# Optimization experiments

Measured on AMD Instinct MI355X. Metric: run time of the kernel, lower is better.

The kernel has to match this reference:

```python
import jax, jax.numpy as jnp
import numpy as np

D_MODEL = 768
N_HEADS = 12
D_K = D_MODEL // N_HEADS
NEG_INF = -1e10


def setup_inputs() -> dict:
    key = jax.random.key(0)
    ks = jax.random.split(key, 12)
    B, S = 2, 4096
    scale = 1.0 / np.sqrt(D_MODEL)
    inp = {
        "q": jax.random.normal(ks[0], (B, S, D_MODEL), jnp.float32),
        "k": jax.random.normal(ks[1], (B, S, D_MODEL), jnp.float32),
        "v": jax.random.normal(ks[2], (B, S, D_MODEL), jnp.float32),
        "mask": jnp.ones((B, S), jnp.int32),
        "Wq": jax.random.normal(ks[3], (D_MODEL, D_MODEL), jnp.float32) * scale,
        "bq": jnp.zeros((D_MODEL,), jnp.float32),
        "Wk": jax.random.normal(ks[4], (D_MODEL, D_MODEL), jnp.float32) * scale,
        "bk": jnp.zeros((D_MODEL,), jnp.float32),
        "Wv": jax.random.normal(ks[5], (D_MODEL, D_MODEL), jnp.float32) * scale,
        "bv": jnp.zeros((D_MODEL,), jnp.float32),
        "Wo": jax.random.normal(ks[6], (D_MODEL, D_MODEL), jnp.float32) * scale,
        "bo": jnp.zeros((D_MODEL,), jnp.float32),
    }
    return inp


def reference(q, k, v, mask, Wq, bq, Wk, bk, Wv, bv, Wo, bo):
    B, Sq, _ = q.shape
    Sk = k.shape[1]
    # linear projections (flax Linear: x @ kernel + bias)
    query = q @ Wq + bq
    key_ = k @ Wk + bk
    value = v @ Wv + bv
    # split heads: [B, H, S, d_k]
    query = query.reshape(B, Sq, N_HEADS, D_K).transpose(0, 2, 1, 3)
    key_ = key_.reshape(B, Sk, N_HEADS, D_K).transpose(0, 2, 1, 3)
    value = value.reshape(B, Sk, N_HEADS, D_K).transpose(0, 2, 1, 3)
    # scores [B, H, Sq, Sk]
    scores = jnp.einsum('bhqd,bhkd->bhqk', query, key_) / jnp.sqrt(
        jnp.asarray(D_K, query.dtype))
    m = mask[:, None, None, :]  # 2D mask -> [B,1,1,Sk]
    scores = jnp.where(m == 0, NEG_INF, scores)
    attn = jax.nn.softmax(scores, axis=-1)
    # dropout deterministic (is_training=False): identity
    x = jnp.einsum('bhqk,bhkd->bhqd', attn, value)
    x = x.transpose(0, 2, 1, 3).reshape(B, Sq, D_MODEL)
    return x @ Wo + bo
```

## Files before the change

### kernel.cpp

```cpp
#include <hip/hip_runtime.h>

typedef __attribute__((ext_vector_type(8))) short short8;
typedef __attribute__((ext_vector_type(4))) float floatx4;
typedef __attribute__((ext_vector_type(16))) float floatx16;
typedef unsigned short ushort_t;

#define S_LEN 4096
#define NH 12
#define DK 64
#define DM 768
#define BQ 128
#define LOG2E 1.4426950408889634f

static __device__ __forceinline__ unsigned short f2bf(float f) {
    unsigned int u = __float_as_uint(f);
    u += 0x7FFFu + ((u >> 16) & 1u);
    return (unsigned short)(u >> 16);
}
static __device__ __forceinline__ unsigned pack2(float a, float b) {
    return (unsigned)f2bf(a) | ((unsigned)f2bf(b) << 16);
}
static __device__ __forceinline__ void gld_lds16(const void* g, void* l) {
    __builtin_amdgcn_global_load_lds(
        (__attribute__((address_space(1))) void*)g,
        (__attribute__((address_space(3))) void*)l, 16, 0, 0);
}

__global__ __launch_bounds__(256)
void wtrans_kernel(const float* __restrict__ W0, const float* __restrict__ W1,
                   const float* __restrict__ W2, const float* __restrict__ W3,
                   ushort_t* __restrict__ T0, ushort_t* __restrict__ T1,
                   ushort_t* __restrict__ T2, ushort_t* __restrict__ T3) {
    __shared__ float tile[32][33];
    const int z = blockIdx.z;
    const float* W = (z == 0) ? W0 : (z == 1) ? W1 : (z == 2) ? W2 : W3;
    ushort_t* T = (z == 0) ? T0 : (z == 1) ? T1 : (z == 2) ? T2 : T3;
    const int bx = blockIdx.x, by = blockIdx.y;
    const int tx = threadIdx.x, ty = threadIdx.y;
    #pragma unroll
    for (int j = 0; j < 32; j += 8)
        tile[ty + j][tx] = W[(size_t)(by * 32 + ty + j) * DM + bx * 32 + tx];
    __syncthreads();
    #pragma unroll
    for (int j = 0; j < 32; j += 8)
        T[(size_t)(bx * 32 + ty + j) * DM + by * 32 + tx] = f2bf(tile[tx][ty + j]);
}

__global__ __launch_bounds__(256)
void cvt_kernel(const float* __restrict__ A0, const float* __restrict__ A1,
                const float* __restrict__ A2, ushort_t* __restrict__ O0,
                ushort_t* __restrict__ O1, ushort_t* __restrict__ O2) {
    const int z = blockIdx.y;
    const float* A = (z == 0) ? A0 : (z == 1) ? A1 : A2;
    ushort_t* O = (z == 0) ? O0 : (z == 1) ? O1 : O2;
    const size_t i = ((size_t)blockIdx.x * 256 + threadIdx.x) * 8;
    const float4 f0 = *(const float4*)(A + i);
    const float4 f1 = *(const float4*)(A + i + 4);
    uint4 o;
    o.x = pack2(f0.x, f0.y);
    o.y = pack2(f0.z, f0.w);
    o.z = pack2(f1.x, f1.y);
    o.w = pack2(f1.z, f1.w);
    *(uint4*)(O + i) = o;
}

__global__ __launch_bounds__(256)
void vtrans_kernel(const ushort_t* __restrict__ Vn, ushort_t* __restrict__ Vt) {
    __shared__ ushort_t tl[64 * 72];
    const int s0 = blockIdx.x * 64;
    const size_t bh = blockIdx.y;
    const int t = threadIdx.x;
    {
        const int r = t >> 2, c0 = (t & 3) * 16;
        const uint4* src = (const uint4*)(Vn + (bh * S_LEN + s0 + r) * DK + c0);
        uint4 a0 = src[0], a1 = src[1];
        uint4* dst = (uint4*)&tl[r * 72 + c0];
        dst[0] = a0;
        dst[1] = a1;
    }
    __syncthreads();
    {
        const int d = t >> 2, c0 = (t & 3) * 16;
        alignas(16) ushort_t tmp[16];
        #pragma unroll
        for (int j = 0; j < 16; ++j) tmp[j] = tl[(c0 + j) * 72 + d];
        uint4* dst = (uint4*)(Vt + (bh * DK + d) * S_LEN + s0 + c0);
        dst[0] = *(const uint4*)&tmp[0];
        dst[1] = *(const uint4*)&tmp[8];
    }
}

struct GemmArgs {
    const ushort_t* A[3];
    const ushort_t* Wt[3];
    const float* bias[3];
    void* C[3];
    float scale[3];
};

template <int MODE>
__global__ __launch_bounds__(256, 3)
void gemm_kernel(GemmArgs args) {
    __shared__ __align__(16) ushort_t As[128 * 64];
    __shared__ __align__(16) ushort_t Bs[128 * 64];
    const int z = blockIdx.z;
    const ushort_t* A = args.A[z];
    const ushort_t* Wt = args.Wt[z];
    const float* bias = args.bias[z];
    void* Carg = args.C[z];
    const float scale = args.scale[z];

    const int m0 = blockIdx.x * 128;
    const int n0 = blockIdx.y * 128;
    const int t = threadIdx.x;
    const int w = t >> 6, lane = t & 63, l15 = lane & 15, quad = lane >> 4;
    const int rowoff = (w >> 1) * 64, coloff = (w & 1) * 64;
    const int srow = w * 8 + (lane >> 3);
    const int schunk = lane & 7;
    const int gchunk = schunk ^ (lane >> 3);

    floatx4 acc[4][4];
    #pragma unroll
    for (int i = 0; i < 4; ++i)
        #pragma unroll
        for (int j = 0; j < 4; ++j) acc[i][j] = (floatx4){0.f, 0.f, 0.f, 0.f};

    for (int kt = 0; kt < DM; kt += 64) {
        __syncthreads();
        #pragma unroll
        for (int j = 0; j < 4; ++j) {
            const int r = j * 32 + srow;
            gld_lds16(A + (size_t)(m0 + r) * DM + kt + gchunk * 8,
                      &As[r * 64 + schunk * 8]);
        }
        #pragma unroll
        for (int j = 0; j < 4; ++j) {
            const int r = j * 32 + srow;
            gld_lds16(Wt + (size_t)(n0 + r) * DM + kt + gchunk * 8,
                      &Bs[r * 64 + schunk * 8]);
        }
        __asm__ __volatile__("s_waitcnt vmcnt(0)" ::: "memory");
        __syncthreads();

        #pragma unroll
        for (int kk = 0; kk < 2; ++kk) {
            short8 af[4], bfr[4];
            #pragma unroll
            for (int i = 0; i < 4; ++i) {
                const int r = rowoff + 16 * i + l15;
                af[i] = *(const short8*)&As[r * 64 + (((kk * 4 + quad) ^ (r & 7)) << 3)];
            }
            #pragma unroll
            for (int j = 0; j < 4; ++j) {
                const int r = coloff + 16 * j + l15;
                bfr[j] = *(const short8*)&Bs[r * 64 + (((kk * 4 + quad) ^ (r & 7)) << 3)];
            }
            #pragma unroll
            for (int i = 0; i < 4; ++i)
                #pragma unroll
                for (int j = 0; j < 4; ++j)
                    acc[i][j] = __builtin_amdgcn_mfma_f32_16x16x32_bf16(af[i], bfr[j], acc[i][j], 0, 0, 0);
        }
    }

    #pragma unroll
    for (int i = 0; i < 4; ++i) {
        #pragma unroll
        for (int j = 0; j < 4; ++j) {
            #pragma unroll
            for (int reg = 0; reg < 4; ++reg) {
                const int m = m0 + rowoff + 16 * i + quad * 4 + reg;
                const int n = n0 + coloff + 16 * j + l15;
                const float v2 = (acc[i][j][reg] + bias[n]) * scale;
                if (MODE == 0) {
                    ushort_t* Out = (ushort_t*)Carg;
                    const int b = m >> 12, s = m & 4095, h = n >> 6, d = n & 63;
                    Out[((size_t)((b * NH + h) * S_LEN + s)) * DK + d] = f2bf(v2);
                } else {
                    float* Out = (float*)Carg;
                    Out[(size_t)m * DM + n] = v2;
                }
            }
        }
    }
}

__global__ __launch_bounds__(256, 3)
void attn_kernel(const ushort_t* __restrict__ Q, const ushort_t* __restrict__ K,
                 const ushort_t* __restrict__ VT, const int* __restrict__ mask,
                 ushort_t* __restrict__ X) {
    __shared__ ushort_t Qs[BQ * DK];
    __shared__ ushort_t Ks0[64 * DK], Ks1[64 * DK];
    __shared__ ushort_t Vs0[64 * DK], Vs1[64 * DK];

    const int id = blockIdx.x;
    const int per = id >> 3;
    const int bh = (id & 7) * 3 + (per >> 5);
    const int qb = per & 31;
    const int b = bh / NH, h = bh - b * NH;
    const size_t bho = (size_t)bh * S_LEN;
    const ushort_t* Vbase = VT + (size_t)bh * DK * S_LEN;
    const int t = threadIdx.x;
    const int w = t >> 6, lane = t & 63, l31 = lane & 31, half = lane >> 5;
    const int q0 = qb * BQ;
    const int swl = l31 & 7;
    const int frow8 = lane >> 3;
    const int fcc = lane & 7;

    auto fillK = [&](int kv0, ushort_t* Kb) {
        #pragma unroll
        for (int j = 0; j < 2; ++j) {
            const int r = (w * 2 + j) * 8 + frow8;
            const int c8 = fcc ^ (r & 7);
            gld_lds16(K + (bho + kv0 + r) * DK + c8 * 8, &Kb[r * DK + fcc * 8]);
        }
    };
    auto fillV = [&](int kv0, ushort_t* Vb) {
        #pragma unroll
        for (int j = 0; j < 2; ++j) {
            const int r = (w * 2 + j) * 8 + frow8;
            const int c8 = fcc ^ (r & 7);
            gld_lds16(Vbase + (size_t)r * S_LEN + kv0 + c8 * 8, &Vb[r * DK + fcc * 8]);
        }
    };

    fillK(0, Ks0);
    fillV(0, Vs0);
    #pragma unroll
    for (int j = 0; j < 4; ++j) {
        const int r = (w * 4 + j) * 8 + frow8;
        const int c8 = fcc ^ (r & 7);
        gld_lds16(Q + (bho + q0 + r) * DK + c8 * 8, &Qs[r * DK + fcc * 8]);
    }
    int ok = 1;
    {
        const int* mrow = mask + (size_t)b * S_LEN + t * 16;
        #pragma unroll
        for (int i = 0; i < 4; ++i) {
            const int4 mm = *(const int4*)(mrow + i * 4);
            ok &= (mm.x != 0) & (mm.y != 0) & (mm.z != 0) & (mm.w != 0);
        }
    }
    const int allones = __syncthreads_and(ok);

    short8 qf[4];
    #pragma unroll
    for (int ks = 0; ks < 4; ++ks) {
        const int c8 = ks * 2 + half;
        qf[ks] = *(const short8*)&Qs[(w * 32 + l31) * DK + ((c8 ^ swl) << 3)];
    }

    floatx16 o[2];
    #pragma unroll
    for (int dt = 0; dt < 2; ++dt)
        #pragma unroll
        for (int r = 0; r < 16; ++r) o[dt][r] = 0.f;
    float l_r = 0.f;

    auto body = [&](int it, const ushort_t* Kc, const ushort_t* Vc,
                    ushort_t* Kn, ushort_t* Vn) {
        __syncthreads();
        if (it + 1 < S_LEN / 64) {
            fillK((it + 1) * 64, Kn);
            fillV((it + 1) * 64, Vn);
        }
        unsigned long long mb = ~0ULL;
        if (!allones) {
            const int mv = mask[(size_t)b * S_LEN + it * 64 + lane];
            mb = __ballot(mv != 0);
        }

        floatx16 st[2];
        __builtin_amdgcn_s_setprio(1);
        #pragma unroll
        for (int kt = 0; kt < 2; ++kt) {
            floatx16 s;
            #pragma unroll
            for (int r = 0; r < 16; ++r) s[r] = 0.f;
            #pragma unroll
            for (int ks = 0; ks < 4; ++ks) {
                const int c8 = ks * 2 + half;
                const short8 kf = *(const short8*)&Kc[(kt * 32 + l31) * DK + ((c8 ^ swl) << 3)];
                s = __builtin_amdgcn_mfma_f32_32x32x16_bf16(kf, qf[ks], s, 0, 0, 0);
            }
            st[kt] = s;
        }
        __builtin_amdgcn_s_setprio(0);

        if (mb != ~0ULL) {
            #pragma unroll
            for (int kt = 0; kt < 2; ++kt) {
                const unsigned bits = (unsigned)(mb >> (kt * 32));
                const unsigned vbits = bits >> (half * 4);
                #pragma unroll
                for (int r = 0; r < 16; ++r)
                    if (!((vbits >> ((r & 3) + 8 * (r >> 2))) & 1)) st[kt][r] = -3.0e10f;
            }
        }

        short8 pf[4];
        #pragma unroll
        for (int kt = 0; kt < 2; ++kt) {
            float p[16];
            #pragma unroll
            for (int r = 0; r < 16; ++r) p[r] = __builtin_amdgcn_exp2f(st[kt][r]);
            #pragma unroll
            for (int g = 0; g < 4; ++g)
                l_r += (p[4 * g + 0] + p[4 * g + 1]) + (p[4 * g + 2] + p[4 * g + 3]);
            unsigned c0[4], c1[4];
            #pragma unroll
            for (int g = 0; g < 4; ++g) {
                asm("v_cvt_pk_bf16_f32 %0, %1, %2"
                    : "=v"(c0[g]) : "v"(p[4 * g + 0]), "v"(p[4 * g + 1]));
                asm("v_cvt_pk_bf16_f32 %0, %1, %2"
                    : "=v"(c1[g]) : "v"(p[4 * g + 2]), "v"(p[4 * g + 3]));
            }
            asm("v_permlane32_swap_b32 %0, %1" : "+v"(c0[0]), "+v"(c0[1]));
            asm("v_permlane32_swap_b32 %0, %1" : "+v"(c1[0]), "+v"(c1[1]));
            asm("v_permlane32_swap_b32 %0, %1" : "+v"(c0[2]), "+v"(c0[3]));
            asm("v_permlane32_swap_b32 %0, %1" : "+v"(c1[2]), "+v"(c1[3]));
            union { short8 s8; unsigned u[4]; } w0, w1;
            w0.u[0] = c0[0]; w0.u[1] = c1[0]; w0.u[2] = c0[1]; w0.u[3] = c1[1];
            w1.u[0] = c0[2]; w1.u[1] = c1[2]; w1.u[2] = c0[3]; w1.u[3] = c1[3];
            pf[kt * 2 + 0] = w0.s8;
            pf[kt * 2 + 1] = w1.s8;
        }

        __builtin_amdgcn_s_setprio(1);
        #pragma unroll
        for (int dt = 0; dt < 2; ++dt) {
            #pragma unroll
            for (int ks = 0; ks < 4; ++ks) {
                const int c8 = ks * 2 + half;
                const short8 vf = *(const short8*)&Vc[(dt * 32 + l31) * DK + ((c8 ^ swl) << 3)];
                o[dt] = __builtin_amdgcn_mfma_f32_32x32x16_bf16(pf[ks], vf, o[dt], 0, 0, 0);
            }
        }
        __builtin_amdgcn_s_setprio(0);
    };

    for (int it = 0; it < S_LEN / 64; it += 2) {
        body(it, Ks0, Vs0, Ks1, Vs1);
        body(it + 1, Ks1, Vs1, Ks0, Vs0);
    }

    l_r += __shfl_xor(l_r, 32);
    const float inv = 1.0f / l_r;
    float iv[16];
    #pragma unroll
    for (int r = 0; r < 16; ++r)
        iv[r] = __shfl(inv, (r & 3) + 8 * (r >> 2) + 4 * half);
    #pragma unroll
    for (int dt = 0; dt < 2; ++dt)
        #pragma unroll
        for (int r = 0; r < 16; ++r) {
            const int qrow = (r & 3) + 8 * (r >> 2) + 4 * half;
            const int s = q0 + w * 32 + qrow;
            const int d = h * DK + dt * 32 + l31;
            X[((size_t)b * S_LEN + s) * DM + d] = f2bf(o[dt][r] * iv[r]);
        }
}

extern "C" void kernel_launch(void* const* d_in, const int* in_sizes, int n_in,
                              void* d_out, int out_size, void* d_ws, size_t ws_size,
                              hipStream_t stream) {
    const float* q = (const float*)d_in[0];
    const float* k = (const float*)d_in[1];
    const float* v = (const float*)d_in[2];
    const int* mask = (const int*)d_in[3];
    const float* Wq = (const float*)d_in[4];
    const float* bq = (const float*)d_in[5];
    const float* Wk = (const float*)d_in[6];
    const float* bk = (const float*)d_in[7];
    const float* Wv = (const float*)d_in[8];
    const float* bv = (const float*)d_in[9];
    const float* Wo = (const float*)d_in[10];
    const float* bo = (const float*)d_in[11];
    float* out = (float*)d_out;

    const size_t ME = (size_t)2 * S_LEN * DM;
    const size_t WE = (size_t)DM * DM;
    ushort_t* Qb = (ushort_t*)d_ws;
    ushort_t* Kb = Qb + ME;
    ushort_t* Vb = Kb + ME;
    ushort_t* VTb = Vb + ME;
    ushort_t* Xb = VTb + ME;
    ushort_t* Wqt = Xb + ME;
    ushort_t* Wkt = Wqt + WE;
    ushort_t* Wvt = Wkt + WE;
    ushort_t* Wot = Wvt + WE;
    ushort_t* Qa = Xb;
    ushort_t* Ka = VTb;
    ushort_t* Va = (ushort_t*)d_out;

    wtrans_kernel<<<dim3(DM / 32, DM / 32, 4), dim3(32, 8), 0, stream>>>(
        Wq, Wk, Wv, Wo, Wqt, Wkt, Wvt, Wot);

    cvt_kernel<<<dim3((int)(ME / 8 / 256), 3), 256, 0, stream>>>(q, k, v, Qa, Ka, Va);

    GemmArgs g1;
    g1.A[0] = Qa;  g1.A[1] = Ka;  g1.A[2] = Va;
    g1.Wt[0] = Wqt; g1.Wt[1] = Wkt; g1.Wt[2] = Wvt;
    g1.bias[0] = bq; g1.bias[1] = bk; g1.bias[2] = bv;
    g1.C[0] = Qb;  g1.C[1] = Kb;  g1.C[2] = Vb;
    g1.scale[0] = 0.125f * LOG2E;
    g1.scale[1] = 1.0f; g1.scale[2] = 1.0f;
    gemm_kernel<0><<<dim3((2 * S_LEN) / 128, DM / 128, 3), 256, 0, stream>>>(g1);

    vtrans_kernel<<<dim3(S_LEN / 64, 2 * NH), 256, 0, stream>>>(Vb, VTb);

    attn_kernel<<<dim3(768), 256, 0, stream>>>(Qb, Kb, VTb, mask, Xb);

    GemmArgs g2;
    g2.A[0] = Xb;  g2.A[1] = Xb;  g2.A[2] = Xb;
    g2.Wt[0] = Wot; g2.Wt[1] = Wot; g2.Wt[2] = Wot;
    g2.bias[0] = bo; g2.bias[1] = bo; g2.bias[2] = bo;
    g2.C[0] = out; g2.C[1] = out; g2.C[2] = out;
    g2.scale[0] = 1.0f; g2.scale[1] = 1.0f; g2.scale[2] = 1.0f;
    gemm_kernel<1><<<dim3((2 * S_LEN) / 128, DM / 128, 1), 256, 0, stream>>>(g2);
}
```

Before: 313.4 us.

## Software-pipeline attention loop: overlap QK softmax of next tile with PV of previous

Restructures the attention main loop so each step computes QK^T and the softmax exponentials for tile i while doing the PV MFMAs for tile i-1. This lets the exp/convert VALU work interleave with matrix work. V uses a triple buffer, with the third buffer aliased onto the Q shared-memory region since Q is already in registers, so LDS use does not grow. The loop is manually unrolled by six with a prologue and epilogue. The cost is more live registers (two P fragment sets) and a more intricate buffer-rotation schedule that could hurt occupancy.

```diff
diff --git a/kernel.cpp b/kernel.cpp
--- a/kernel.cpp
+++ b/kernel.cpp
@@ -189,9 +189,13 @@
 void attn_kernel(const ushort_t* __restrict__ Q, const ushort_t* __restrict__ K,
                  const ushort_t* __restrict__ VT, const int* __restrict__ mask,
                  ushort_t* __restrict__ X) {
-    __shared__ ushort_t Qs[BQ * DK];
-    __shared__ ushort_t Ks0[64 * DK], Ks1[64 * DK];
-    __shared__ ushort_t Vs0[64 * DK], Vs1[64 * DK];
+    __shared__ ushort_t smem[BQ * DK + 4 * 64 * DK];
+    ushort_t* Qs = smem;
+    ushort_t* Vs2 = smem;
+    ushort_t* Ks0 = smem + BQ * DK;
+    ushort_t* Ks1 = Ks0 + 64 * DK;
+    ushort_t* Vs0 = Ks1 + 64 * DK;
+    ushort_t* Vs1 = Vs0 + 64 * DK;
 
     const int id = blockIdx.x;
     const int per = id >> 3;
@@ -256,20 +260,14 @@
         #pragma unroll
         for (int r = 0; r < 16; ++r) o[dt][r] = 0.f;
     float l_r = 0.f;
-
-    auto body = [&](int it, const ushort_t* Kc, const ushort_t* Vc,
-                    ushort_t* Kn, ushort_t* Vn) {
-        __syncthreads();
-        if (it + 1 < S_LEN / 64) {
-            fillK((it + 1) * 64, Kn);
-            fillV((it + 1) * 64, Vn);
-        }
+    short8 pfA[4], pfB[4];
+
+    auto qk_softmax = [&](int it, const ushort_t* Kc, short8* pfc) {
         unsigned long long mb = ~0ULL;
         if (!allones) {
             const int mv = mask[(size_t)b * S_LEN + it * 64 + lane];
             mb = __ballot(mv != 0);
         }
-
         floatx16 st[2];
         __builtin_amdgcn_s_setprio(1);
         #pragma unroll
@@ -298,7 +296,6 @@
             }
         }
 
-        short8 pf[4];
         #pragma unroll
         for (int kt = 0; kt < 2; ++kt) {
             float p[16];
@@ -322,27 +319,58 @@
             union { short8 s8; unsigned u[4]; } w0, w1;
             w0.u[0] = c0[0]; w0.u[1] = c1[0]; w0.u[2] = c0[1]; w0.u[3] = c1[1];
             w1.u[0] = c0[2]; w1.u[1] = c1[2]; w1.u[2] = c0[3]; w1.u[3] = c1[3];
-            pf[kt * 2 + 0] = w0.s8;
-            pf[kt * 2 + 1] = w1.s8;
-        }
-
+            pfc[kt * 2 + 0] = w0.s8;
+            pfc[kt * 2 + 1] = w1.s8;
+        }
+    };
+
+    auto pv = [&](const ushort_t* Vp, const short8* pfp) {
         __builtin_amdgcn_s_setprio(1);
         #pragma unroll
         for (int dt = 0; dt < 2; ++dt) {
             #pragma unroll
             for (int ks = 0; ks < 4; ++ks) {
                 const int c8 = ks * 2 + half;
-                const short8 vf = *(const short8*)&Vc[(dt * 32 + l31) * DK + ((c8 ^ swl) << 3)];
-                o[dt] = __builtin_amdgcn_mfma_f32_32x32x16_bf16(pf[ks], vf, o[dt], 0, 0, 0);
+                const short8 vf = *(const short8*)&Vp[(dt * 32 + l31) * DK + ((c8 ^ swl) << 3)];
+                o[dt] = __builtin_amdgcn_mfma_f32_32x32x16_bf16(pfp[ks], vf, o[dt], 0, 0, 0);
             }
         }
         __builtin_amdgcn_s_setprio(0);
     };
 
-    for (int it = 0; it < S_LEN / 64; it += 2) {
-        body(it, Ks0, Vs0, Ks1, Vs1);
-        body(it + 1, Ks1, Vs1, Ks0, Vs0);
-    }
+    fillK(64, Ks1);
+    fillV(64, Vs1);
+    qk_softmax(0, Ks0, pfA);
+
+    for (int itb = 1; itb <= 55; itb += 6) {
+        __syncthreads();
+        fillK((itb + 1) * 64, Ks0); fillV((itb + 1) * 64, Vs2);
+        qk_softmax(itb + 0, Ks1, pfB); pv(Vs0, pfA);
+        __syncthreads();
+        fillK((itb + 2) * 64, Ks1); fillV((itb + 2) * 64, Vs0);
+        qk_softmax(itb + 1, Ks0, pfA); pv(Vs1, pfB);
+        __syncthreads();
+        fillK((itb + 3) * 64, Ks0); fillV((itb + 3) * 64, Vs1);
+        qk_softmax(itb + 2, Ks1, pfB); pv(Vs2, pfA);
+        __syncthreads();
+        fillK((itb + 4) * 64, Ks1); fillV((itb + 4) * 64, Vs2);
+        qk_softmax(itb + 3, Ks0, pfA); pv(Vs0, pfB);
+        __syncthreads();
+        fillK((itb + 5) * 64, Ks0); fillV((itb + 5) * 64, Vs0);
+        qk_softmax(itb + 4, Ks1, pfB); pv(Vs1, pfA);
+        __syncthreads();
+        fillK((itb + 6) * 64, Ks1); fillV((itb + 6) * 64, Vs1);
+        qk_softmax(itb + 5, Ks0, pfA); pv(Vs2, pfB);
+    }
+    __syncthreads();
+    fillK(62 * 64, Ks0); fillV(62 * 64, Vs2);
+    qk_softmax(61, Ks1, pfB); pv(Vs0, pfA);
+    __syncthreads();
+    fillK(63 * 64, Ks1); fillV(63 * 64, Vs0);
+    qk_softmax(62, Ks0, pfA); pv(Vs1, pfB);
+    __syncthreads();
+    qk_softmax(63, Ks1, pfB); pv(Vs2, pfA);
+    pv(Vs0, pfB);
 
     l_r += __shfl_xor(l_r, 32);
     const float inv = 1.0f / l_r;
```

After: 597.3 us. +90.6%, slower.
